# Kernel tuning notes

Measured on AMD Instinct MI355X. Metric: run time of the kernel, lower is better.

## Reference

```python
import jax, jax.numpy as jnp
import numpy as np

DIM = 768
NUM_HEADS = 12
HEAD_DIM = DIM // NUM_HEADS
SCALE = HEAD_DIM ** -0.5
B, N = 8, 1024


def setup_inputs() -> dict:
    key = jax.random.key(0)
    k1, k2, k3, k4, k5 = jax.random.split(key, 5)
    x = jax.random.normal(k1, (B, N, DIM), dtype=jnp.float32)
    # qkv: Linear(dim, 3*dim, bias=False); proj: Linear(dim, dim) with bias
    w_qkv = jax.random.normal(k2, (3 * DIM, DIM), dtype=jnp.float32) * (DIM ** -0.5)
    w_proj = jax.random.normal(k3, (DIM, DIM), dtype=jnp.float32) * (DIM ** -0.5)
    b_proj = jnp.zeros((DIM,), dtype=jnp.float32)
    # learned attention mask parameter, shape (H, L, L) with L >= N
    att_mask = jax.random.normal(k4, (NUM_HEADS, N, N), dtype=jnp.float32)
    return {"x": x, "w_qkv": w_qkv, "w_proj": w_proj, "b_proj": b_proj, "att_mask": att_mask}


def reference(x, w_qkv, w_proj, b_proj, att_mask):
    Bx, Nx, C = x.shape
    # qkv projection -> (3, B, H, N, head_dim)
    qkv = (x @ w_qkv.T).reshape(Bx, Nx, 3, NUM_HEADS, C // NUM_HEADS)
    qkv = jnp.transpose(qkv, (2, 0, 3, 1, 4))
    q, k, v = qkv[0], qkv[1], qkv[2]  # gpd_ratio==active_ratio==1 -> scaling factor 1
    # scores [B, H, N, N]
    attn = jnp.einsum('bhnd,bhmd->bhnm', q, k) * SCALE
    # custom sigmoid mask gating before softmax (broadcast over batch)
    attn = attn * jax.nn.sigmoid(att_mask[:, :Nx, :Nx])[None, :, :, :]
    attn = jax.nn.softmax(attn, axis=-1)
    out = jnp.einsum('bhnm,bhmd->bhnd', attn, v)
    out = jnp.transpose(out, (0, 2, 1, 3)).reshape(Bx, Nx, C)
    return out @ w_proj.T + b_proj
```

## Files before the change

### kernel.cpp

```cpp
#include <hip/hip_runtime.h>
#include <math.h>
#include <stdint.h>

typedef unsigned short u16;
typedef __attribute__((ext_vector_type(8))) short short8;
typedef __attribute__((ext_vector_type(4))) float f32x4;

#define GATE_SCALE 0.18033688011112042f

#if __has_builtin(__builtin_amdgcn_exp2f)
#define FEXP2(x) __builtin_amdgcn_exp2f(x)
#else
#define FEXP2(x) exp2f(x)
#endif

__device__ __forceinline__ u16 f2b(float f) {
    union { float f; unsigned u; } v; v.f = f;
    unsigned r = v.u + 0x7fffu + ((v.u >> 16) & 1u);
    return (u16)(r >> 16);
}
__device__ __forceinline__ u16 f2b_hu(float f) {
    union { float f; unsigned u; } v; v.f = f;
    return (u16)((v.u + 0x8000u) >> 16);
}
__device__ __forceinline__ float b2f(u16 u) {
    union { float f; unsigned u; } v; v.u = ((unsigned)u) << 16; return v.f;
}

#define GLL16(gsrc, ldsbase) __builtin_amdgcn_global_load_lds(                    \
    (__attribute__((address_space(1))) void*)(uintptr_t)(gsrc),                   \
    (__attribute__((address_space(3))) void*)(uint32_t)(uintptr_t)(ldsbase),      \
    16, 0, 0)

#define NX4  1572864
#define NW14 442368
#define NW24 147456
#define NXW4 (NX4 + NW14 + NW24)

__global__ __launch_bounds__(256) void prep_xw(
    const float4* __restrict__ x, const float4* __restrict__ wq,
    const float4* __restrict__ wp,
    ushort4* __restrict__ xb, ushort4* __restrict__ wqb,
    ushort4* __restrict__ wpb)
{
    size_t i = (size_t)blockIdx.x * 256 + threadIdx.x;
    float4 v; ushort4* dst; size_t j;
    if (i < NX4)            { j = i;               v = x[j];  dst = xb;  }
    else if (i < NX4 + NW14){ j = i - NX4;         v = wq[j]; dst = wqb; }
    else                    { j = i - (NX4 + NW14);v = wp[j]; dst = wpb; }
    ushort4 o; o.x = f2b(v.x); o.y = f2b(v.y); o.z = f2b(v.z); o.w = f2b(v.w);
    dst[j] = o;
}

__global__ __launch_bounds__(256) void prep_gate(
    const float4* __restrict__ mask4, u16* __restrict__ gp)
{
    __shared__ u16 L[64][72];
    const int bid = blockIdx.x;
    const int kt = bid & 15, qt = (bid >> 4) & 15, h = bid >> 8;
    const int t = threadIdx.x;

    #pragma unroll
    for (int s = 0; s < 4; ++s) {
        const int idx = t + s * 256;
        const int row = idx >> 4, c4 = idx & 15;
        float4 v = mask4[(size_t)(h * 1024 + qt * 64 + row) * 256 + kt * 16 + c4];
        L[row][c4 * 4 + 0] = f2b(GATE_SCALE / (1.f + __expf(-v.x)));
        L[row][c4 * 4 + 1] = f2b(GATE_SCALE / (1.f + __expf(-v.y)));
        L[row][c4 * 4 + 2] = f2b(GATE_SCALE / (1.f + __expf(-v.z)));
        L[row][c4 * 4 + 3] = f2b(GATE_SCALE / (1.f + __expf(-v.w)));
    }
    __syncthreads();

    const int w = t >> 6, l = t & 63;
    const int fq = l >> 4, fr = l & 15;
    union { u16 u[16]; float4 f[2]; } vals;
    #pragma unroll
    for (int i = 0; i < 4; ++i)
        #pragma unroll
        for (int nt = 0; nt < 4; ++nt)
            vals.u[i * 4 + nt] = L[16 * w + 4 * fq + i][nt * 16 + fr];
    float4* dst = (float4*)(gp + (size_t)bid * 4096 + (size_t)t * 16);
    dst[0] = vals.f[0];
    dst[1] = vals.f[1];
}

__global__ __launch_bounds__(256) void qkv_gemm(
    const u16* __restrict__ xb, const u16* __restrict__ wb,
    u16* __restrict__ qb, u16* __restrict__ kb, u16* __restrict__ vb)
{
    __shared__ u16 As[3][4096];
    __shared__ u16 Bs[3][4096];
    const int t = threadIdx.x, l = t & 63, w = t >> 6;
    const int wm = (w & 1) * 64, wn = (w >> 1) * 64;

    const int orig = blockIdx.x + 18 * blockIdx.y;
    const int nid = (orig & 7) * 144 + (orig >> 3);
    const int m0 = (nid / 18) * 128, c0 = (nid % 18) * 128;

    f32x4 acc[4][4];
    #pragma unroll
    for (int i = 0; i < 4; ++i)
        #pragma unroll
        for (int j = 0; j < 4; ++j) { f32x4 z = {0.f,0.f,0.f,0.f}; acc[i][j] = z; }

    const int srow = l >> 2, sseg = l & 3;
    const int gcol = ((sseg ^ ((srow >> 1) & 3)) << 3);
    const u16* a0 = xb + (size_t)(m0 + w * 16 + srow) * 768 + gcol;
    const u16* a1 = a0 + (size_t)64 * 768;
    const u16* b0p = wb + (size_t)(c0 + w * 16 + srow) * 768 + gcol;
    const u16* b1p = b0p + (size_t)64 * 768;
    const int wofs = w * 512;

    const int fr = l & 15, fq = l >> 4;
    const int fseg = (fq ^ ((fr >> 1) & 3)) << 3;

    auto stage = [&](int bi, int koff) {
        GLL16(a0 + koff, &As[bi][wofs]);
        GLL16(a1 + koff, &As[bi][2048 + wofs]);
        GLL16(b0p + koff, &Bs[bi][wofs]);
        GLL16(b1p + koff, &Bs[bi][2048 + wofs]);
    };

    stage(0, 0);
    stage(1, 32);

    int cur = 0;
    for (int kt = 0; kt < 24; ++kt) {
        if (kt < 23) asm volatile("s_waitcnt vmcnt(4)" ::: "memory");
        else         asm volatile("s_waitcnt vmcnt(0)" ::: "memory");
        __builtin_amdgcn_s_barrier();
        if (kt < 22) {
            const int nn = (cur == 0) ? 2 : cur - 1;
            stage(nn, (kt + 2) * 32);
        }
        const u16* A = As[cur];
        const u16* B = Bs[cur];
        short8 af[4], bf[4];
        #pragma unroll
        for (int mt = 0; mt < 4; ++mt)
            af[mt] = *(const short8*)&A[(wm + mt * 16 + fr) * 32 + fseg];
        #pragma unroll
        for (int nt = 0; nt < 4; ++nt)
            bf[nt] = *(const short8*)&B[(wn + nt * 16 + fr) * 32 + fseg];
        #pragma unroll
        for (int mt = 0; mt < 4; ++mt)
            #pragma unroll
            for (int nt = 0; nt < 4; ++nt)
                acc[mt][nt] = __builtin_amdgcn_mfma_f32_16x16x32_bf16(
                    af[mt], bf[nt], acc[mt][nt], 0, 0, 0);
        cur = (cur == 2) ? 0 : cur + 1;
    }

    const int b = m0 >> 10;
    const int n0 = m0 & 1023;
    #pragma unroll
    for (int nt = 0; nt < 4; ++nt) {
        const int c = c0 + wn + nt * 16 + fr;
        const int which = c / 768;
        const int rem = c - which * 768;
        const int h = rem >> 6, d = rem & 63;
        if (which < 2) {
            u16* dst = ((which == 0) ? qb : kb)
                       + ((size_t)(b * 12 + h) * 1024) * 64 + d;
            #pragma unroll
            for (int mt = 0; mt < 4; ++mt)
                #pragma unroll
                for (int r = 0; r < 4; ++r) {
                    const int n = n0 + wm + mt * 16 + fq * 4 + r;
                    dst[(size_t)n * 64] = f2b(acc[mt][nt][r]);
                }
        } else {
            u16* dst = vb + ((size_t)(b * 12 + h) * 64 + d) * 1024
                          + n0 + wm + fq * 4;
            #pragma unroll
            for (int mt = 0; mt < 4; ++mt) {
                ushort4 pk;
                pk.x = f2b(acc[mt][nt][0]); pk.y = f2b(acc[mt][nt][1]);
                pk.z = f2b(acc[mt][nt][2]); pk.w = f2b(acc[mt][nt][3]);
                *(ushort4*)(dst + mt * 16) = pk;
            }
        }
    }
}

__global__ __launch_bounds__(256, 3) void flash_attn(
    const u16* __restrict__ qb, const u16* __restrict__ kb,
    const u16* __restrict__ vt, const u16* __restrict__ gperm,
    u16* __restrict__ aob)
{
    __shared__ u16 Qs[8192], Ks[4096], Vts[4096], Ps[4096];
    const int t = threadIdx.x, l = t & 63, w = t >> 6;
    const int bid = blockIdx.x;
    const int qtb = bid & 7, bh = bid >> 3;
    const int h = bh % 12, b = bh / 12;
    const int q0 = qtb * 128;

    const u16* hq = qb + (size_t)bh * 65536;
    const u16* hk = kb + (size_t)bh * 65536;
    const u16* hv = vt + (size_t)bh * 65536;
    const u16* hgb = gperm + ((size_t)h * 256 + qtb * 32) * 4096 + (w * 64 + l) * 16;

    const int sr = l >> 3, ss = l & 7;
    const int sg = ((ss ^ (sr & 7)) << 3);
    const int j0 = w * 2, j1 = j0 + 1;

    #pragma unroll
    for (int jq = 0; jq < 4; ++jq) {
        const int j = w * 4 + jq;
        GLL16(hq + (size_t)(q0 + j * 8 + sr) * 64 + sg, Qs + j * 512);
    }
    GLL16(hk + (size_t)(j0 * 8 + sr) * 64 + sg, Ks + j0 * 512);
    GLL16(hk + (size_t)(j1 * 8 + sr) * 64 + sg, Ks + j1 * 512);
    GLL16(hv + (size_t)(j0 * 8 + sr) * 1024 + sg, Vts + j0 * 512);
    GLL16(hv + (size_t)(j1 * 8 + sr) * 1024 + sg, Vts + j1 * 512);
    __syncthreads();

    const int fq = l >> 4, fr = l & 15;
    const int sega = ((fq ^ (fr & 7)) << 3);
    const int segb = (((4 + fq) ^ (fr & 7)) << 3);

    short8 aq[2][2];
    #pragma unroll
    for (int qh = 0; qh < 2; ++qh) {
        const int row = 16 * w + fr;
        aq[qh][0] = *(const short8*)&Qs[qh * 4096 + row * 64 + sega];
        aq[qh][1] = *(const short8*)&Qs[qh * 4096 + row * 64 + segb];
    }

    short8 gn[4];
    gn[0] = *(const short8*)(hgb);
    gn[1] = *(const short8*)(hgb + 8);
    gn[2] = *(const short8*)(hgb + 65536);
    gn[3] = *(const short8*)(hgb + 65536 + 8);

    float l_part[2][4] = {{0.f,0.f,0.f,0.f},{0.f,0.f,0.f,0.f}};
    f32x4 o[2][4];
    #pragma unroll
    for (int qh = 0; qh < 2; ++qh)
        #pragma unroll
        for (int nt = 0; nt < 4; ++nt) { f32x4 z = {0.f,0.f,0.f,0.f}; o[qh][nt] = z; }

    for (int kt = 0; kt < 16; ++kt) {
        short8 g[4];
        #pragma unroll
        for (int s = 0; s < 4; ++s) g[s] = gn[s];
        if (kt < 15) {
            const size_t go = (size_t)(kt + 1) * 4096;
            gn[0] = *(const short8*)(hgb + go);
            gn[1] = *(const short8*)(hgb + go + 8);
            gn[2] = *(const short8*)(hgb + 65536 + go);
            gn[3] = *(const short8*)(hgb + 65536 + go + 8);
        }

        f32x4 sv[2][4];
        #pragma unroll
        for (int nt = 0; nt < 4; ++nt) {
            short8 kf0 = *(const short8*)&Ks[(nt * 16 + fr) * 64 + sega];
            short8 kf1 = *(const short8*)&Ks[(nt * 16 + fr) * 64 + segb];
            f32x4 z0 = {0.f,0.f,0.f,0.f};
            z0 = __builtin_amdgcn_mfma_f32_16x16x32_bf16(aq[0][0], kf0, z0, 0, 0, 0);
            z0 = __builtin_amdgcn_mfma_f32_16x16x32_bf16(aq[0][1], kf1, z0, 0, 0, 0);
            sv[0][nt] = z0;
            f32x4 z1 = {0.f,0.f,0.f,0.f};
            z1 = __builtin_amdgcn_mfma_f32_16x16x32_bf16(aq[1][0], kf0, z1, 0, 0, 0);
            z1 = __builtin_amdgcn_mfma_f32_16x16x32_bf16(aq[1][1], kf1, z1, 0, 0, 0);
            sv[1][nt] = z1;
        }

        short8 ap[2][2];
        #pragma unroll
        for (int qh = 0; qh < 2; ++qh) {
            #pragma unroll
            for (int i = 0; i < 4; ++i) {
                const int pr = 4 * fq + i;
                #pragma unroll
                for (int nt = 0; nt < 4; ++nt) {
                    const int idx = i * 4 + nt;
                    const float gv = b2f((u16)(idx < 8 ? g[2 * qh][idx]
                                                       : g[2 * qh + 1][idx - 8]));
                    const float p = FEXP2(sv[qh][nt][i] * gv);
                    l_part[qh][i] += p;
                    const int col = nt * 16 + fr;
                    Ps[w * 1024 + pr * 64 + (((col >> 3) ^ (pr & 7)) << 3) + (col & 7)]
                        = f2b_hu(p);
                }
            }
            ap[qh][0] = *(const short8*)&Ps[w * 1024 + fr * 64 + sega];
            ap[qh][1] = *(const short8*)&Ps[w * 1024 + fr * 64 + segb];
        }

        #pragma unroll
        for (int nt = 0; nt < 4; ++nt) {
            short8 vf0 = *(const short8*)&Vts[(nt * 16 + fr) * 64 + sega];
            short8 vf1 = *(const short8*)&Vts[(nt * 16 + fr) * 64 + segb];
            o[0][nt] = __builtin_amdgcn_mfma_f32_16x16x32_bf16(ap[0][0], vf0, o[0][nt], 0, 0, 0);
            o[0][nt] = __builtin_amdgcn_mfma_f32_16x16x32_bf16(ap[0][1], vf1, o[0][nt], 0, 0, 0);
            o[1][nt] = __builtin_amdgcn_mfma_f32_16x16x32_bf16(ap[1][0], vf0, o[1][nt], 0, 0, 0);
            o[1][nt] = __builtin_amdgcn_mfma_f32_16x16x32_bf16(ap[1][1], vf1, o[1][nt], 0, 0, 0);
        }

        if (kt < 15) {
            __syncthreads();
            const size_t ko = (size_t)(kt + 1) * 64;
            GLL16(hk + (ko + j0 * 8 + sr) * 64 + sg, Ks + j0 * 512);
            GLL16(hk + (ko + j1 * 8 + sr) * 64 + sg, Ks + j1 * 512);
            GLL16(hv + (size_t)(j0 * 8 + sr) * 1024 + ko + sg, Vts + j0 * 512);
            GLL16(hv + (size_t)(j1 * 8 + sr) * 1024 + ko + sg, Vts + j1 * 512);
            __syncthreads();
        }
    }

    #pragma unroll
    for (int qh = 0; qh < 2; ++qh) {
        #pragma unroll
        for (int i = 0; i < 4; ++i) {
            float s = l_part[qh][i];
            s += __shfl_xor(s, 1, 16);
            s += __shfl_xor(s, 2, 16);
            s += __shfl_xor(s, 4, 16);
            s += __shfl_xor(s, 8, 16);
            const float inv = 1.f / s;
            const int n = q0 + qh * 64 + 16 * w + 4 * fq + i;
            const size_t rowoff = ((size_t)b * 1024 + n) * 768 + h * 64;
            #pragma unroll
            for (int nt = 0; nt < 4; ++nt)
                aob[rowoff + nt * 16 + fr] = f2b(o[qh][nt][i] * inv);
        }
    }
}

__global__ __launch_bounds__(256) void proj_gemm(
    const u16* __restrict__ aob, const u16* __restrict__ wb,
    const float* __restrict__ bproj, float* __restrict__ out)
{
    __shared__ u16 As[3][4096];
    __shared__ u16 Bs[3][4096];
    const int t = threadIdx.x, l = t & 63, w = t >> 6;
    const int wm = (w & 1) * 64, wn = (w >> 1) * 64;

    const int orig = blockIdx.x + 6 * blockIdx.y;
    const int nid = (orig & 7) * 48 + (orig >> 3);
    const int m0 = (nid / 6) * 128, c0 = (nid % 6) * 128;

    f32x4 acc[4][4];
    #pragma unroll
    for (int i = 0; i < 4; ++i)
        #pragma unroll
        for (int j = 0; j < 4; ++j) { f32x4 z = {0.f,0.f,0.f,0.f}; acc[i][j] = z; }

    const int srow = l >> 2, sseg = l & 3;
    const int gcol = ((sseg ^ ((srow >> 1) & 3)) << 3);
    const u16* a0 = aob + (size_t)(m0 + w * 16 + srow) * 768 + gcol;
    const u16* a1 = a0 + (size_t)64 * 768;
    const u16* b0p = wb + (size_t)(c0 + w * 16 + srow) * 768 + gcol;
    const u16* b1p = b0p + (size_t)64 * 768;
    const int wofs = w * 512;

    const int fr = l & 15, fq = l >> 4;
    const int fseg = (fq ^ ((fr >> 1) & 3)) << 3;

    auto stage = [&](int bi, int koff) {
        GLL16(a0 + koff, &As[bi][wofs]);
        GLL16(a1 + koff, &As[bi][2048 + wofs]);
        GLL16(b0p + koff, &Bs[bi][wofs]);
        GLL16(b1p + koff, &Bs[bi][2048 + wofs]);
    };

    stage(0, 0);
    stage(1, 32);

    int cur = 0;
    for (int kt = 0; kt < 24; ++kt) {
        if (kt < 23) asm volatile("s_waitcnt vmcnt(4)" ::: "memory");
        else         asm volatile("s_waitcnt vmcnt(0)" ::: "memory");
        __builtin_amdgcn_s_barrier();
        if (kt < 22) {
            const int nn = (cur == 0) ? 2 : cur - 1;
            stage(nn, (kt + 2) * 32);
        }
        const u16* A = As[cur];
        const u16* B = Bs[cur];
        short8 af[4], bf[4];
        #pragma unroll
        for (int mt = 0; mt < 4; ++mt)
            af[mt] = *(const short8*)&A[(wm + mt * 16 + fr) * 32 + fseg];
        #pragma unroll
        for (int nt = 0; nt < 4; ++nt)
            bf[nt] = *(const short8*)&B[(wn + nt * 16 + fr) * 32 + fseg];
        #pragma unroll
        for (int mt = 0; mt < 4; ++mt)
            #pragma unroll
            for (int nt = 0; nt < 4; ++nt)
                acc[mt][nt] = __builtin_amdgcn_mfma_f32_16x16x32_bf16(
                    af[mt], bf[nt], acc[mt][nt], 0, 0, 0);
        cur = (cur == 2) ? 0 : cur + 1;
    }

    #pragma unroll
    for (int nt = 0; nt < 4; ++nt) {
        const int c = c0 + wn + nt * 16 + fr;
        const float bias = bproj[c];
        #pragma unroll
        for (int mt = 0; mt < 4; ++mt)
            #pragma unroll
            for (int r = 0; r < 4; ++r) {
                const int m = m0 + wm + mt * 16 + fq * 4 + r;
                out[(size_t)m * 768 + c] = acc[mt][nt][r] + bias;
            }
    }
}

extern "C" void kernel_launch(void* const* d_in, const int* in_sizes, int n_in,
                              void* d_out, int out_size, void* d_ws, size_t ws_size,
                              hipStream_t stream)
{
    const float* x     = (const float*)d_in[0];
    const float* wqkv  = (const float*)d_in[1];
    const float* wproj = (const float*)d_in[2];
    const float* bproj = (const float*)d_in[3];
    const float* mask  = (const float*)d_in[4];
    float* out = (float*)d_out;

    char* ws = (char*)d_ws;
    u16* gperm  = (u16*)(ws);
    u16* xb     = (u16*)(ws + 25165824);
    u16* wqkvb  = (u16*)(ws + 37748736);
    u16* wprojb = (u16*)(ws + 41287680);
    u16* qb     = (u16*)(ws + 42467328);
    u16* kb     = (u16*)(ws + 55050240);
    u16* vb     = (u16*)(ws + 67633152);
    u16* aob    = (u16*)(ws + 80216064);

    prep_xw<<<NXW4 / 256, 256, 0, stream>>>(
        (const float4*)x, (const float4*)wqkv, (const float4*)wproj,
        (ushort4*)xb, (ushort4*)wqkvb, (ushort4*)wprojb);

    prep_gate<<<3072, 256, 0, stream>>>((const float4*)mask, gperm);

    qkv_gemm<<<dim3(18, 64), 256, 0, stream>>>(xb, wqkvb, qb, kb, vb);

    flash_attn<<<768, 256, 0, stream>>>(qb, kb, vb, gperm, aob);

    proj_gemm<<<dim3(6, 64), 256, 0, stream>>>(aob, wprojb, bproj, out);
}
```

Before: 242.5 us.

## Double-buffer K/V tiles in flash attention and fuse prep kernels

The flash attention kernel now double-buffers K and V tiles in LDS. The next tile's async global-to-LDS loads are issued at the top of each iteration, guarded by a vmcnt wait and a single barrier, replacing two syncthreads per iteration. Q fragments are read straight from global memory into registers instead of being staged through LDS, which frees shared memory and lets the launch bound rise to 4 blocks per CU. The two prep kernels are merged into one launch to save a kernel launch. The vmcnt(4) count relies on the gate loads and GLL ordering being exactly as assumed, and direct Q global loads are uncoalesced per lane.

```diff
diff --git a/kernel.cpp b/kernel.cpp
--- a/kernel.cpp
+++ b/kernel.cpp
@@ -37,28 +37,30 @@
 #define NW24 147456
 #define NXW4 (NX4 + NW14 + NW24)
 
-__global__ __launch_bounds__(256) void prep_xw(
+__global__ __launch_bounds__(256) void prep_all(
     const float4* __restrict__ x, const float4* __restrict__ wq,
     const float4* __restrict__ wp,
     ushort4* __restrict__ xb, ushort4* __restrict__ wqb,
-    ushort4* __restrict__ wpb)
-{
-    size_t i = (size_t)blockIdx.x * 256 + threadIdx.x;
-    float4 v; ushort4* dst; size_t j;
-    if (i < NX4)            { j = i;               v = x[j];  dst = xb;  }
-    else if (i < NX4 + NW14){ j = i - NX4;         v = wq[j]; dst = wqb; }
-    else                    { j = i - (NX4 + NW14);v = wp[j]; dst = wpb; }
-    ushort4 o; o.x = f2b(v.x); o.y = f2b(v.y); o.z = f2b(v.z); o.w = f2b(v.w);
-    dst[j] = o;
-}
-
-__global__ __launch_bounds__(256) void prep_gate(
+    ushort4* __restrict__ wpb,
     const float4* __restrict__ mask4, u16* __restrict__ gp)
 {
     __shared__ u16 L[64][72];
-    const int bid = blockIdx.x;
+    const int bx = blockIdx.x;
+    const int t = threadIdx.x;
+
+    if (bx >= 3072) {
+        size_t i = (size_t)(bx - 3072) * 256 + t;
+        float4 v; ushort4* dst; size_t j;
+        if (i < NX4)            { j = i;               v = x[j];  dst = xb;  }
+        else if (i < NX4 + NW14){ j = i - NX4;         v = wq[j]; dst = wqb; }
+        else                    { j = i - (NX4 + NW14);v = wp[j]; dst = wpb; }
+        ushort4 o; o.x = f2b(v.x); o.y = f2b(v.y); o.z = f2b(v.z); o.w = f2b(v.w);
+        dst[j] = o;
+        return;
+    }
+
+    const int bid = bx;
     const int kt = bid & 15, qt = (bid >> 4) & 15, h = bid >> 8;
-    const int t = threadIdx.x;
 
     #pragma unroll
     for (int s = 0; s < 4; ++s) {
@@ -184,12 +186,12 @@
     }
 }
 
-__global__ __launch_bounds__(256, 3) void flash_attn(
+__global__ __launch_bounds__(256, 4) void flash_attn(
     const u16* __restrict__ qb, const u16* __restrict__ kb,
     const u16* __restrict__ vt, const u16* __restrict__ gperm,
     u16* __restrict__ aob)
 {
-    __shared__ u16 Qs[8192], Ks[4096], Vts[4096], Ps[4096];
+    __shared__ u16 Ks[2][4096], Vts[2][4096], Ps[4096];
     const int t = threadIdx.x, l = t & 63, w = t >> 6;
     const int bid = blockIdx.x;
     const int qtb = bid & 7, bh = bid >> 3;
@@ -205,17 +207,6 @@
     const int sg = ((ss ^ (sr & 7)) << 3);
     const int j0 = w * 2, j1 = j0 + 1;
 
-    #pragma unroll
-    for (int jq = 0; jq < 4; ++jq) {
-        const int j = w * 4 + jq;
-        GLL16(hq + (size_t)(q0 + j * 8 + sr) * 64 + sg, Qs + j * 512);
-    }
-    GLL16(hk + (size_t)(j0 * 8 + sr) * 64 + sg, Ks + j0 * 512);
-    GLL16(hk + (size_t)(j1 * 8 + sr) * 64 + sg, Ks + j1 * 512);
-    GLL16(hv + (size_t)(j0 * 8 + sr) * 1024 + sg, Vts + j0 * 512);
-    GLL16(hv + (size_t)(j1 * 8 + sr) * 1024 + sg, Vts + j1 * 512);
-    __syncthreads();
-
     const int fq = l >> 4, fr = l & 15;
     const int sega = ((fq ^ (fr & 7)) << 3);
     const int segb = (((4 + fq) ^ (fr & 7)) << 3);
@@ -223,10 +214,16 @@
     short8 aq[2][2];
     #pragma unroll
     for (int qh = 0; qh < 2; ++qh) {
-        const int row = 16 * w + fr;
-        aq[qh][0] = *(const short8*)&Qs[qh * 4096 + row * 64 + sega];
-        aq[qh][1] = *(const short8*)&Qs[qh * 4096 + row * 64 + segb];
-    }
+        const u16* qrow = hq + (size_t)(q0 + qh * 64 + 16 * w + fr) * 64;
+        aq[qh][0] = *(const short8*)(qrow + fq * 8);
+        aq[qh][1] = *(const short8*)(qrow + 32 + fq * 8);
+    }
+
+    GLL16(hk + (size_t)(j0 * 8 + sr) * 64 + sg, &Ks[0][j0 * 512]);
+    GLL16(hk + (size_t)(j1 * 8 + sr) * 64 + sg, &Ks[0][j1 * 512]);
+    GLL16(hv + (size_t)(j0 * 8 + sr) * 1024 + sg, &Vts[0][j0 * 512]);
+    GLL16(hv + (size_t)(j1 * 8 + sr) * 1024 + sg, &Vts[0][j1 * 512]);
+    __builtin_amdgcn_sched_barrier(0);
 
     short8 gn[4];
     gn[0] = *(const short8*)(hgb);
@@ -242,6 +239,20 @@
         for (int nt = 0; nt < 4; ++nt) { f32x4 z = {0.f,0.f,0.f,0.f}; o[qh][nt] = z; }
 
     for (int kt = 0; kt < 16; ++kt) {
+        asm volatile("s_waitcnt vmcnt(4)" ::: "memory");
+        __builtin_amdgcn_s_barrier();
+
+        if (kt < 15) {
+            const size_t ko = (size_t)(kt + 1) * 64;
+            u16* kd = &Ks[(kt + 1) & 1][0];
+            u16* vd = &Vts[(kt + 1) & 1][0];
+            GLL16(hk + (ko + j0 * 8 + sr) * 64 + sg, kd + j0 * 512);
+            GLL16(hk + (ko + j1 * 8 + sr) * 64 + sg, kd + j1 * 512);
+            GLL16(hv + (size_t)(j0 * 8 + sr) * 1024 + ko + sg, vd + j0 * 512);
+            GLL16(hv + (size_t)(j1 * 8 + sr) * 1024 + ko + sg, vd + j1 * 512);
+            __builtin_amdgcn_sched_barrier(0);
+        }
+
         short8 g[4];
         #pragma unroll
         for (int s = 0; s < 4; ++s) g[s] = gn[s];
@@ -253,11 +264,14 @@
             gn[3] = *(const short8*)(hgb + 65536 + go + 8);
         }
 
+        const u16* KS = &Ks[kt & 1][0];
+        const u16* VS = &Vts[kt & 1][0];
+
         f32x4 sv[2][4];
         #pragma unroll
         for (int nt = 0; nt < 4; ++nt) {
-            short8 kf0 = *(const short8*)&Ks[(nt * 16 + fr) * 64 + sega];
-            short8 kf1 = *(const short8*)&Ks[(nt * 16 + fr) * 64 + segb];
+            short8 kf0 = *(const short8*)&KS[(nt * 16 + fr) * 64 + sega];
+            short8 kf1 = *(const short8*)&KS[(nt * 16 + fr) * 64 + segb];
             f32x4 z0 = {0.f,0.f,0.f,0.f};
             z0 = __builtin_amdgcn_mfma_f32_16x16x32_bf16(aq[0][0], kf0, z0, 0, 0, 0);
             z0 = __builtin_amdgcn_mfma_f32_16x16x32_bf16(aq[0][1], kf1, z0, 0, 0, 0);
@@ -292,22 +306,12 @@
 
         #pragma unroll
         for (int nt = 0; nt < 4; ++nt) {
-            short8 vf0 = *(const short8*)&Vts[(nt * 16 + fr) * 64 + sega];
-            short8 vf1 = *(const short8*)&Vts[(nt * 16 + fr) * 64 + segb];
+            short8 vf0 = *(const short8*)&VS[(nt * 16 + fr) * 64 + sega];
+            short8 vf1 = *(const short8*)&VS[(nt * 16 + fr) * 64 + segb];
             o[0][nt] = __builtin_amdgcn_mfma_f32_16x16x32_bf16(ap[0][0], vf0, o[0][nt], 0, 0, 0);
             o[0][nt] = __builtin_amdgcn_mfma_f32_16x16x32_bf16(ap[0][1], vf1, o[0][nt], 0, 0, 0);
             o[1][nt] = __builtin_amdgcn_mfma_f32_16x16x32_bf16(ap[1][0], vf0, o[1][nt], 0, 0, 0);
             o[1][nt] = __builtin_amdgcn_mfma_f32_16x16x32_bf16(ap[1][1], vf1, o[1][nt], 0, 0, 0);
-        }
-
-        if (kt < 15) {
-            __syncthreads();
-            const size_t ko = (size_t)(kt + 1) * 64;
-            GLL16(hk + (ko + j0 * 8 + sr) * 64 + sg, Ks + j0 * 512);
-            GLL16(hk + (ko + j1 * 8 + sr) * 64 + sg, Ks + j1 * 512);
-            GLL16(hv + (size_t)(j0 * 8 + sr) * 1024 + ko + sg, Vts + j0 * 512);
-            GLL16(hv + (size_t)(j1 * 8 + sr) * 1024 + ko + sg, Vts + j1 * 512);
-            __syncthreads();
         }
     }
 
@@ -432,11 +436,10 @@
     u16* vb     = (u16*)(ws + 67633152);
     u16* aob    = (u16*)(ws + 80216064);
 
-    prep_xw<<<NXW4 / 256, 256, 0, stream>>>(
+    prep_all<<<3072 + NXW4 / 256, 256, 0, stream>>>(
         (const float4*)x, (const float4*)wqkv, (const float4*)wproj,
-        (ushort4*)xb, (ushort4*)wqkvb, (ushort4*)wprojb);
-
-    prep_gate<<<3072, 256, 0, stream>>>((const float4*)mask, gperm);
+        (ushort4*)xb, (ushort4*)wqkvb, (ushort4*)wprojb,
+        (const float4*)mask, gperm);
 
     qkv_gemm<<<dim3(18, 64), 256, 0, stream>>>(xb, wqkvb, qb, kb, vb);
 
```

After: 326.3 us. 34.6% more time.
